# Kernel tuning notes

Measured on AMD Instinct MI355X. Metric: run time of the kernel, lower is better.

The kernel has to match this reference:

```python
import jax, jax.numpy as jnp
import numpy as np

N_NODES = 50000
N_EDGES = 800000
F_IN = 64
HID = 64
N_CLASSES = 10
N_GRAPHS = 64


def setup_inputs() -> dict:
    key = jax.random.key(0)
    ks = jax.random.split(key, 16)
    x = jax.random.normal(ks[0], (N_NODES, F_IN), dtype=jnp.float32)
    edge_index = jax.random.randint(ks[1], (2, N_EDGES), 0, N_NODES, dtype=jnp.int32)
    supernode_mask = jax.random.bernoulli(ks[2], 0.1, (N_NODES,))
    edge_mask = jax.random.bernoulli(ks[3], 0.5, (N_EDGES,)).astype(jnp.float32)
    batch = jnp.sort(jax.random.randint(ks[4], (N_NODES,), 0, N_GRAPHS, dtype=jnp.int32))
    def glorot(k, fan_in, fan_out):
        s = jnp.sqrt(6.0 / (fan_in + fan_out))
        return jax.random.uniform(k, (fan_in, fan_out), jnp.float32, -s, s)
    W1 = glorot(ks[5], F_IN, HID); b1 = jnp.zeros((HID,), jnp.float32)
    W2 = glorot(ks[6], HID, HID); b2 = jnp.zeros((HID,), jnp.float32)
    W3 = glorot(ks[7], HID, HID); b3 = jnp.zeros((HID,), jnp.float32)
    Wl = glorot(ks[8], HID, N_CLASSES); bl = jnp.zeros((N_CLASSES,), jnp.float32)
    return {"x": x, "edge_index": edge_index, "supernode_mask": supernode_mask,
            "edge_mask": edge_mask, "batch": batch,
            "W1": W1, "b1": b1, "W2": W2, "b2": b2, "W3": W3, "b3": b3,
            "Wl": Wl, "bl": bl}


def reference(x, edge_index, supernode_mask, edge_mask, batch,
              W1, b1, W2, b2, W3, b3, Wl, bl):
    N = x.shape[0]
    src, dst = edge_index[0], edge_index[1]

    # SimpleConv('add'): weighted sum of source features into targets
    x2 = jax.ops.segment_sum(x[src] * edge_mask[:, None], dst, num_segments=N)
    x = jnp.where(supernode_mask[:, None], x2, x)

    # GCN normalization with self-loops: deg = 1 + in-degree, norm = d^-1/2[src]*d^-1/2[dst]
    deg = jax.ops.segment_sum(jnp.ones((src.shape[0],), x.dtype), dst, num_segments=N) + 1.0
    dinv = jax.lax.rsqrt(deg)
    coef = dinv[src] * dinv[dst]          # [E]
    self_coef = (dinv * dinv)[:, None]    # self-loop contribution [N,1]

    def gcn(h, W, b):
        h = h @ W  # small GEMM [N, HID]
        agg = jax.ops.segment_sum(h[src] * coef[:, None], dst, num_segments=N)
        return agg + h * self_coef + b

    h = jax.nn.relu(gcn(x, W1, b1))
    h = jax.nn.relu(gcn(h, W2, b2))
    h = gcn(h, W3, b3)

    # global_mean_pool over graphs
    sums = jax.ops.segment_sum(h, batch, num_segments=N_GRAPHS)
    cnt = jax.ops.segment_sum(jnp.ones((N,), h.dtype), batch, num_segments=N_GRAPHS)
    pooled = sums / jnp.maximum(cnt, 1.0)[:, None]

    # dropout is identity in eval mode
    return pooled @ Wl + bl
```

## Files before the change

kernel.cpp:

```cpp
#include <hip/hip_runtime.h>

#define FEAT 64
#define NGRAPH 64
#define POOL_CHUNKS 8


__device__ __forceinline__ unsigned int pack_bf16(float a, float b) {
    unsigned int ua = __float_as_uint(a), ub = __float_as_uint(b);
    ua = (ua + 0x7FFFu + ((ua >> 16) & 1u)) >> 16;
    ub = (ub + 0x7FFFu + ((ub >> 16) & 1u)) >> 16;
    return ua | (ub << 16);
}
__device__ __forceinline__ float bf_lo(unsigned int w) {
    return __uint_as_float(w << 16);
}
__device__ __forceinline__ float bf_hi(unsigned int w) {
    return __uint_as_float(w & 0xFFFF0000u);
}

__global__ __launch_bounds__(256) void k_init(int* __restrict__ cnt_int,
                                              float* __restrict__ pooled,
                                              int* __restrict__ flag, int N) {
    int i = blockIdx.x * 256 + threadIdx.x;
    if (i < N) cnt_int[i] = 0;
    if (i < NGRAPH * FEAT) pooled[i] = 0.f;
    if (i == 0) *flag = 0;
}

__global__ __launch_bounds__(256) void k_detect(const unsigned int* __restrict__ m,
                                                int nwords, int* __restrict__ flag) {
    int i = blockIdx.x * 256 + threadIdx.x;
    if (i >= nwords) return;
    unsigned int w = m[i];
    if (w == 0x3F800000u) atomicOr(flag, 2);
    else if (w > 1u) atomicOr(flag, 1);
}

__device__ __forceinline__ bool read_mask(const void* sm, int i, int fl) {
    if (fl & 2) return ((const float*)sm)[i] != 0.f;
    if (fl & 1) return ((const unsigned char*)sm)[i] != 0;
    return ((const int*)sm)[i] != 0;
}

__global__ __launch_bounds__(256) void k_count(const int* __restrict__ ei,
                                               int* __restrict__ cnt_int,
                                               int* __restrict__ rank, int E) {
    int e = blockIdx.x * 256 + threadIdx.x;
    if (e >= E) return;
    rank[e] = atomicAdd(&cnt_int[ei[E + e]], 1);
}

__global__ __launch_bounds__(256) void k_scan1(const int* __restrict__ cnt,
                                               int* __restrict__ rowptr,
                                               int* __restrict__ bsum, int N) {
    __shared__ int woff[4];
    int t = threadIdx.x, lane = t & 63, wid = t >> 6;
    int i = blockIdx.x * 256 + t;
    int orig = (i < N) ? cnt[i] : 0;
    int v = orig;
#pragma unroll
    for (int off = 1; off < 64; off <<= 1) {
        int u = __shfl_up(v, off);
        if (lane >= off) v += u;
    }
    if (lane == 63) woff[wid] = v;
    __syncthreads();
    if (t == 0) {
        int a = 0;
#pragma unroll
        for (int w = 0; w < 4; ++w) { int b = woff[w]; woff[w] = a; a += b; }
    }
    __syncthreads();
    int excl = woff[wid] + v - orig;
    if (i < N) rowptr[i] = excl;
    if (t == 255) bsum[blockIdx.x] = woff[3] + v;
}

__global__ __launch_bounds__(256) void k_scan2(int* __restrict__ bsum, int nb) {
    __shared__ int woff[4];
    int t = threadIdx.x, lane = t & 63, wid = t >> 6;
    int orig = (t < nb) ? bsum[t] : 0;
    int v = orig;
#pragma unroll
    for (int off = 1; off < 64; off <<= 1) {
        int u = __shfl_up(v, off);
        if (lane >= off) v += u;
    }
    if (lane == 63) woff[wid] = v;
    __syncthreads();
    if (t == 0) {
        int a = 0;
#pragma unroll
        for (int w = 0; w < 4; ++w) { int b = woff[w]; woff[w] = a; a += b; }
    }
    __syncthreads();
    if (t < nb) bsum[t] = woff[wid] + v - orig;
}

__global__ __launch_bounds__(256) void k_scan3(const int* __restrict__ cnt,
                                               const int* __restrict__ bsum,
                                               int* __restrict__ rowptr,
                                               float* __restrict__ dinv,
                                               int N, int E) {
    int i = blockIdx.x * 256 + threadIdx.x;
    if (i >= N) return;
    rowptr[i] += bsum[blockIdx.x];
    dinv[i] = rsqrtf((float)cnt[i] + 1.0f);
    if (i == 0) rowptr[N] = E;
}

__global__ __launch_bounds__(256) void k_fill(const int* __restrict__ ei,
                                              const float* __restrict__ emask,
                                              const int* __restrict__ rowptr,
                                              const int* __restrict__ rank,
                                              unsigned int* __restrict__ csr, int E) {
    int e = blockIdx.x * 256 + threadIdx.x;
    if (e >= E) return;
    int dst = ei[E + e];
    unsigned int word = (unsigned int)ei[e];
    if (emask[e] != 0.f) word |= 0x10000u;
    csr[rowptr[dst] + rank[e]] = word;
}

__global__ __launch_bounds__(256) void k_sup(const float* __restrict__ x,
                                             const int* __restrict__ rowptr,
                                             const unsigned int* __restrict__ csr,
                                             const void* __restrict__ sm,
                                             const int* __restrict__ flag,
                                             float* __restrict__ xbuf, int N) {
    int t = blockIdx.x * 256 + threadIdx.x;
    int i = t >> 6, lane = t & 63;
    if (i >= N) return;
    int g = lane >> 4, q = lane & 15;
    int fl = *flag;
    if (read_mask(sm, i, fl)) {
        int r0 = rowptr[i], r1 = rowptr[i + 1];
        float4 acc = {0.f, 0.f, 0.f, 0.f};
        for (int j0 = r0; j0 < r1; j0 += 64) {
            int cnt = min(64, r1 - j0);
            unsigned int w_l = (lane < cnt) ? csr[j0 + lane] : 0u;
            int rounds4 = (cnt + 3) & ~3;
#pragma unroll 2
            for (int j = 0; j < rounds4; j += 4) {
                unsigned int wd = __shfl(w_l, j + g);
                if (wd & 0x10000u) {
                    int s = (int)(wd & 0xFFFFu);
                    const float4 v = *(const float4*)(x + (size_t)s * FEAT + q * 4);
                    acc.x += v.x; acc.y += v.y; acc.z += v.z; acc.w += v.w;
                }
            }
        }
#pragma unroll
        for (int m = 16; m < 64; m <<= 1) {
            acc.x += __shfl_xor(acc.x, m);
            acc.y += __shfl_xor(acc.y, m);
            acc.z += __shfl_xor(acc.z, m);
            acc.w += __shfl_xor(acc.w, m);
        }
        if (g == 0)
            *(float4*)(xbuf + (size_t)i * FEAT + q * 4) = acc;
    } else if (g == 0) {
        const float4 v = *(const float4*)(x + (size_t)i * FEAT + q * 4);
        *(float4*)(xbuf + (size_t)i * FEAT + q * 4) = v;
    }
}

__global__ __launch_bounds__(256) void k_gemm(const float* __restrict__ in,
                                              const float* __restrict__ W,
                                              const float* __restrict__ dinv,
                                              unsigned int* __restrict__ hd, int N) {
    __shared__ float wl[64 * 64];
    __shared__ float xl[16 * 68];
    int t = threadIdx.x;
    int row0 = blockIdx.x * 16;
#pragma unroll
    for (int i = 0; i < 16; ++i) wl[t + i * 256] = W[t + i * 256];
    int r = t >> 4, c = t & 15;
    int row = row0 + r;
    if (row < N)
        *(float4*)(xl + r * 68 + c * 4) = *(const float4*)(in + row * 64 + c * 4);
    __syncthreads();
    if (row >= N) return;
    float4 acc = {0.f, 0.f, 0.f, 0.f};
#pragma unroll
    for (int k = 0; k < 64; ++k) {
        float xv = xl[r * 68 + k];
        const float4 wv = *(const float4*)(wl + k * 64 + c * 4);
        acc.x += xv * wv.x;
        acc.y += xv * wv.y;
        acc.z += xv * wv.z;
        acc.w += xv * wv.w;
    }
    float di = dinv[row];
    uint2 p;
    p.x = pack_bf16(acc.x * di, acc.y * di);
    p.y = pack_bf16(acc.z * di, acc.w * di);
    *(uint2*)(hd + (size_t)row * 32 + c * 2) = p;
}

__global__ __launch_bounds__(256) void k_gather(const unsigned int* __restrict__ hd,
                                                const float* __restrict__ b,
                                                const float* __restrict__ dinv,
                                                const int* __restrict__ rowptr,
                                                const unsigned int* __restrict__ csr,
                                                float* __restrict__ out,
                                                int N, int do_relu) {
    int t = blockIdx.x * 256 + threadIdx.x;
    int i = t >> 6, lane = t & 63;
    if (i >= N) return;
    int g = lane >> 4, q = lane & 15;
    int r0 = rowptr[i], r1 = rowptr[i + 1];
    float4 acc = {0.f, 0.f, 0.f, 0.f};
    for (int j0 = r0; j0 < r1; j0 += 64) {
        int cnt = min(64, r1 - j0);
        int s_l = (lane < cnt) ? (int)(csr[j0 + lane] & 0xFFFFu) : 0;
        int rounds4 = (cnt + 3) & ~3;
#pragma unroll 4
        for (int j = 0; j < rounds4; j += 4) {
            int jj = j + g;
            int s = __shfl(s_l, jj);
            if (jj < cnt) {
                const uint2 v = *(const uint2*)(hd + (size_t)s * 32 + q * 2);
                acc.x += bf_lo(v.x); acc.y += bf_hi(v.x);
                acc.z += bf_lo(v.y); acc.w += bf_hi(v.y);
            }
        }
    }
#pragma unroll
    for (int m = 16; m < 64; m <<= 1) {
        acc.x += __shfl_xor(acc.x, m);
        acc.y += __shfl_xor(acc.y, m);
        acc.z += __shfl_xor(acc.z, m);
        acc.w += __shfl_xor(acc.w, m);
    }
    if (g == 0) {
        float dd = dinv[i];
        const uint2 hv = *(const uint2*)(hd + (size_t)i * 32 + q * 2);
        const float4 bv = *(const float4*)(b + q * 4);
        float4 r;
        r.x = (acc.x + bf_lo(hv.x)) * dd + bv.x;
        r.y = (acc.y + bf_hi(hv.x)) * dd + bv.y;
        r.z = (acc.z + bf_lo(hv.y)) * dd + bv.z;
        r.w = (acc.w + bf_hi(hv.y)) * dd + bv.w;
        if (do_relu) {
            r.x = fmaxf(r.x, 0.f); r.y = fmaxf(r.y, 0.f);
            r.z = fmaxf(r.z, 0.f); r.w = fmaxf(r.w, 0.f);
        }
        *(float4*)(out + (size_t)i * FEAT + q * 4) = r;
    }
}

__device__ __forceinline__ int lbound(const int* a, int n, int key) {
    int lo = 0, hi = n;
    while (lo < hi) {
        int mid = (lo + hi) >> 1;
        if (a[mid] < key) lo = mid + 1; else hi = mid;
    }
    return lo;
}

__global__ __launch_bounds__(256) void k_pool(const float* __restrict__ xbuf,
                                              const int* __restrict__ batch,
                                              float* __restrict__ pooled,
                                              float* __restrict__ gcnt, int N) {
    int g = blockIdx.x >> 3, c = blockIdx.x & (POOL_CHUNKS - 1);
    int lo = lbound(batch, N, g);
    int hi = lbound(batch, N, g + 1);
    int len = hi - lo;
    int t = threadIdx.x, lane = t & 63, sub = t >> 6;
    if (c == 0 && t == 0) gcnt[g] = (float)len;
    int a = lo + (int)(((long long)len * c) / POOL_CHUNKS);
    int bnd = lo + (int)(((long long)len * (c + 1)) / POOL_CHUNKS);
    float s = 0.f;
    for (int i = a + sub; i < bnd; i += 4) s += xbuf[(size_t)i * FEAT + lane];
    __shared__ float red[4][64];
    red[sub][lane] = s;
    __syncthreads();
    if (sub == 0) {
        float tot = red[0][lane] + red[1][lane] + red[2][lane] + red[3][lane];
        unsafeAtomicAdd(&pooled[g * FEAT + lane], tot);
    }
}

__global__ __launch_bounds__(640) void k_logits(const float* __restrict__ pooled,
                                                const float* __restrict__ gcnt,
                                                const float* __restrict__ Wl,
                                                const float* __restrict__ bl,
                                                float* __restrict__ out) {
    int t = threadIdx.x;
    if (t >= NGRAPH * 10) return;
    int g = t / 10, cls = t % 10;
    float inv = 1.f / fmaxf(gcnt[g], 1.f);
    float s = 0.f;
#pragma unroll
    for (int f = 0; f < 64; ++f) s += pooled[g * 64 + f] * Wl[f * 10 + cls];
    out[t] = s * inv + bl[cls];
}

extern "C" void kernel_launch(void* const* d_in, const int* in_sizes, int n_in,
                              void* d_out, int out_size, void* d_ws, size_t ws_size,
                              hipStream_t stream) {
    const float* x = (const float*)d_in[0];
    const int* ei = (const int*)d_in[1];
    const void* sm = d_in[2];
    const float* emask = (const float*)d_in[3];
    const int* batch = (const int*)d_in[4];
    const float* W1 = (const float*)d_in[5];
    const float* b1 = (const float*)d_in[6];
    const float* W2 = (const float*)d_in[7];
    const float* b2 = (const float*)d_in[8];
    const float* W3 = (const float*)d_in[9];
    const float* b3 = (const float*)d_in[10];
    const float* Wl = (const float*)d_in[11];
    const float* bl = (const float*)d_in[12];

    const int N = in_sizes[0] / FEAT;
    const int E = in_sizes[1] / 2;

    float* wsf = (float*)d_ws;
    size_t off = 0;
    float* xbuf = wsf + off;          off += (size_t)N * FEAT;
    unsigned int* hd = (unsigned int*)(wsf + off); off += (size_t)N * 32;
    int* rowptr = (int*)(wsf + off);  off += N + 1;
    int* rank = (int*)(wsf + off);    off += E;
    int* cnt_int = (int*)(wsf + off); off += N;
    float* dinv = wsf + off;          off += N;
    int* bsum = (int*)(wsf + off);    off += 256;
    unsigned int* csr = (unsigned int*)(wsf + off); off += E;
    float* pooled = wsf + off;        off += NGRAPH * FEAT;
    float* gcnt = wsf + off;          off += NGRAPH;
    int* flag = (int*)(wsf + off);

    const int nblocks = (N + 255) / 256;
    const int eblocks = (E + 255) / 256;
    const int wblocks = (N * 64 + 255) / 256;
    const int gemm_blocks = (N + 15) / 16;
    const int detect_blocks = (N / 4 + 255) / 256;

    k_init<<<nblocks, 256, 0, stream>>>(cnt_int, pooled, flag, N);
    k_detect<<<detect_blocks, 256, 0, stream>>>((const unsigned int*)sm, N / 4, flag);
    k_count<<<eblocks, 256, 0, stream>>>(ei, cnt_int, rank, E);
    k_scan1<<<nblocks, 256, 0, stream>>>(cnt_int, rowptr, bsum, N);
    k_scan2<<<1, 256, 0, stream>>>(bsum, nblocks);
    k_scan3<<<nblocks, 256, 0, stream>>>(cnt_int, bsum, rowptr, dinv, N, E);
    k_fill<<<eblocks, 256, 0, stream>>>(ei, emask, rowptr, rank, csr, E);
    k_sup<<<wblocks, 256, 0, stream>>>(x, rowptr, csr, sm, flag, xbuf, N);

    k_gemm<<<gemm_blocks, 256, 0, stream>>>(xbuf, W1, dinv, hd, N);
    k_gather<<<wblocks, 256, 0, stream>>>(hd, b1, dinv, rowptr, csr, xbuf, N, 1);
    k_gemm<<<gemm_blocks, 256, 0, stream>>>(xbuf, W2, dinv, hd, N);
    k_gather<<<wblocks, 256, 0, stream>>>(hd, b2, dinv, rowptr, csr, xbuf, N, 1);
    k_gemm<<<gemm_blocks, 256, 0, stream>>>(xbuf, W3, dinv, hd, N);
    k_gather<<<wblocks, 256, 0, stream>>>(hd, b3, dinv, rowptr, csr, xbuf, N, 0);

    k_pool<<<NGRAPH * POOL_CHUNKS, 256, 0, stream>>>(xbuf, batch, pooled, gcnt, N);
    k_logits<<<1, 640, 0, stream>>>(pooled, gcnt, Wl, bl, (float*)d_out);
}
```

Baseline: 224.9 us.

## Fuse GEMM into gather by aggregating before transform, persistent layer kernel

Uses linearity, A(XW) = (AX)W, to aggregate dinv-scaled bf16 features first and then multiply by W inside the same kernel, with W held in registers per lane. This removes the three separate GEMM kernels and their intermediate round-trips through global memory. The supernode kernel now writes dinv-scaled bf16 input directly, and each layer's output is written as the next layer's prescaled bf16 input. Layers run as a grid-stride persistent kernel with 2048 blocks. The 64-float register array per lane raises register pressure, and the final matvec for every node goes through LDS.

```diff
diff --git a/kernel.cpp b/kernel.cpp
--- a/kernel.cpp
+++ b/kernel.cpp
@@ -3,6 +3,7 @@
 #define FEAT 64
 #define NGRAPH 64
 #define POOL_CHUNKS 8
+#define LAYER_BLOCKS 2048
 
 
 __device__ __forceinline__ unsigned int pack_bf16(float a, float b) {
@@ -127,15 +128,17 @@
                                              const unsigned int* __restrict__ csr,
                                              const void* __restrict__ sm,
                                              const int* __restrict__ flag,
-                                             float* __restrict__ xbuf, int N) {
+                                             const float* __restrict__ dinv,
+                                             unsigned int* __restrict__ u, int N) {
     int t = blockIdx.x * 256 + threadIdx.x;
     int i = t >> 6, lane = t & 63;
     if (i >= N) return;
     int g = lane >> 4, q = lane & 15;
     int fl = *flag;
+    float4 acc;
     if (read_mask(sm, i, fl)) {
         int r0 = rowptr[i], r1 = rowptr[i + 1];
-        float4 acc = {0.f, 0.f, 0.f, 0.f};
+        acc.x = 0.f; acc.y = 0.f; acc.z = 0.f; acc.w = 0.f;
         for (int j0 = r0; j0 < r1; j0 += 64) {
             int cnt = min(64, r1 - j0);
             unsigned int w_l = (lane < cnt) ? csr[j0 + lane] : 0u;
@@ -157,96 +160,83 @@
             acc.z += __shfl_xor(acc.z, m);
             acc.w += __shfl_xor(acc.w, m);
         }
-        if (g == 0)
-            *(float4*)(xbuf + (size_t)i * FEAT + q * 4) = acc;
-    } else if (g == 0) {
-        const float4 v = *(const float4*)(x + (size_t)i * FEAT + q * 4);
-        *(float4*)(xbuf + (size_t)i * FEAT + q * 4) = v;
-    }
-}
-
-__global__ __launch_bounds__(256) void k_gemm(const float* __restrict__ in,
-                                              const float* __restrict__ W,
-                                              const float* __restrict__ dinv,
-                                              unsigned int* __restrict__ hd, int N) {
-    __shared__ float wl[64 * 64];
-    __shared__ float xl[16 * 68];
-    int t = threadIdx.x;
-    int row0 = blockIdx.x * 16;
-#pragma unroll
-    for (int i = 0; i < 16; ++i) wl[t + i * 256] = W[t + i * 256];
-    int r = t >> 4, c = t & 15;
-    int row = row0 + r;
-    if (row < N)
-        *(float4*)(xl + r * 68 + c * 4) = *(const float4*)(in + row * 64 + c * 4);
-    __syncthreads();
-    if (row >= N) return;
-    float4 acc = {0.f, 0.f, 0.f, 0.f};
-#pragma unroll
-    for (int k = 0; k < 64; ++k) {
-        float xv = xl[r * 68 + k];
-        const float4 wv = *(const float4*)(wl + k * 64 + c * 4);
-        acc.x += xv * wv.x;
-        acc.y += xv * wv.y;
-        acc.z += xv * wv.z;
-        acc.w += xv * wv.w;
-    }
-    float di = dinv[row];
-    uint2 p;
-    p.x = pack_bf16(acc.x * di, acc.y * di);
-    p.y = pack_bf16(acc.z * di, acc.w * di);
-    *(uint2*)(hd + (size_t)row * 32 + c * 2) = p;
-}
-
-__global__ __launch_bounds__(256) void k_gather(const unsigned int* __restrict__ hd,
-                                                const float* __restrict__ b,
-                                                const float* __restrict__ dinv,
-                                                const int* __restrict__ rowptr,
-                                                const unsigned int* __restrict__ csr,
-                                                float* __restrict__ out,
-                                                int N, int do_relu) {
-    int t = blockIdx.x * 256 + threadIdx.x;
-    int i = t >> 6, lane = t & 63;
-    if (i >= N) return;
-    int g = lane >> 4, q = lane & 15;
-    int r0 = rowptr[i], r1 = rowptr[i + 1];
-    float4 acc = {0.f, 0.f, 0.f, 0.f};
-    for (int j0 = r0; j0 < r1; j0 += 64) {
-        int cnt = min(64, r1 - j0);
-        int s_l = (lane < cnt) ? (int)(csr[j0 + lane] & 0xFFFFu) : 0;
-        int rounds4 = (cnt + 3) & ~3;
-#pragma unroll 4
-        for (int j = 0; j < rounds4; j += 4) {
-            int jj = j + g;
-            int s = __shfl(s_l, jj);
-            if (jj < cnt) {
-                const uint2 v = *(const uint2*)(hd + (size_t)s * 32 + q * 2);
-                acc.x += bf_lo(v.x); acc.y += bf_hi(v.x);
-                acc.z += bf_lo(v.y); acc.w += bf_hi(v.y);
-            }
-        }
-    }
-#pragma unroll
-    for (int m = 16; m < 64; m <<= 1) {
-        acc.x += __shfl_xor(acc.x, m);
-        acc.y += __shfl_xor(acc.y, m);
-        acc.z += __shfl_xor(acc.z, m);
-        acc.w += __shfl_xor(acc.w, m);
+    } else {
+        acc = *(const float4*)(x + (size_t)i * FEAT + q * 4);
     }
     if (g == 0) {
         float dd = dinv[i];
-        const uint2 hv = *(const uint2*)(hd + (size_t)i * 32 + q * 2);
-        const float4 bv = *(const float4*)(b + q * 4);
-        float4 r;
-        r.x = (acc.x + bf_lo(hv.x)) * dd + bv.x;
-        r.y = (acc.y + bf_hi(hv.x)) * dd + bv.y;
-        r.z = (acc.z + bf_lo(hv.y)) * dd + bv.z;
-        r.w = (acc.w + bf_hi(hv.y)) * dd + bv.w;
-        if (do_relu) {
-            r.x = fmaxf(r.x, 0.f); r.y = fmaxf(r.y, 0.f);
-            r.z = fmaxf(r.z, 0.f); r.w = fmaxf(r.w, 0.f);
-        }
-        *(float4*)(out + (size_t)i * FEAT + q * 4) = r;
+        uint2 p;
+        p.x = pack_bf16(acc.x * dd, acc.y * dd);
+        p.y = pack_bf16(acc.z * dd, acc.w * dd);
+        *(uint2*)(u + (size_t)i * 32 + q * 2) = p;
+    }
+}
+
+__global__ __launch_bounds__(256, 4) void k_layer(const unsigned int* __restrict__ u,
+                                                  const float* __restrict__ W,
+                                                  const float* __restrict__ bias,
+                                                  const float* __restrict__ dinv,
+                                                  const int* __restrict__ rowptr,
+                                                  const unsigned int* __restrict__ csr,
+                                                  unsigned int* __restrict__ u_out,
+                                                  float* __restrict__ h_out,
+                                                  int N, int mode) {
+    __shared__ float s_lds[4][64];
+    int t = threadIdx.x, lane = t & 63, wid = t >> 6;
+    int g = lane >> 4, q = lane & 15;
+    float w[64];
+#pragma unroll
+    for (int k = 0; k < 64; ++k) w[k] = W[k * 64 + lane];
+    float bl_ = bias[lane];
+    for (int i = blockIdx.x * 4 + wid; i < N; i += LAYER_BLOCKS * 4) {
+        int r0 = rowptr[i], r1 = rowptr[i + 1];
+        float4 acc = {0.f, 0.f, 0.f, 0.f};
+        if (g == 0) {
+            const uint2 v = *(const uint2*)(u + (size_t)i * 32 + q * 2);
+            acc.x += bf_lo(v.x); acc.y += bf_hi(v.x);
+            acc.z += bf_lo(v.y); acc.w += bf_hi(v.y);
+        }
+        for (int j0 = r0; j0 < r1; j0 += 64) {
+            int cnt = min(64, r1 - j0);
+            int s_l = (lane < cnt) ? (int)(csr[j0 + lane] & 0xFFFFu) : 0;
+            int rounds4 = (cnt + 3) & ~3;
+#pragma unroll 4
+            for (int j = 0; j < rounds4; j += 4) {
+                int jj = j + g;
+                int s = __shfl(s_l, jj);
+                if (jj < cnt) {
+                    const uint2 v = *(const uint2*)(u + (size_t)s * 32 + q * 2);
+                    acc.x += bf_lo(v.x); acc.y += bf_hi(v.x);
+                    acc.z += bf_lo(v.y); acc.w += bf_hi(v.y);
+                }
+            }
+        }
+#pragma unroll
+        for (int m = 16; m < 64; m <<= 1) {
+            acc.x += __shfl_xor(acc.x, m);
+            acc.y += __shfl_xor(acc.y, m);
+            acc.z += __shfl_xor(acc.z, m);
+            acc.w += __shfl_xor(acc.w, m);
+        }
+        if (g == 0) *(float4*)(&s_lds[wid][q * 4]) = acc;
+        float y = 0.f;
+#pragma unroll
+        for (int k4 = 0; k4 < 16; ++k4) {
+            const float4 sv = *(const float4*)(&s_lds[wid][k4 * 4]);
+            y += sv.x * w[k4 * 4 + 0] + sv.y * w[k4 * 4 + 1] +
+                 sv.z * w[k4 * 4 + 2] + sv.w * w[k4 * 4 + 3];
+        }
+        float dd = dinv[i];
+        y = y * dd + bl_;
+        if (mode == 0) {
+            y = fmaxf(y, 0.f);
+            float up = y * dd;
+            float other = __shfl_xor(up, 1);
+            if ((lane & 1) == 0)
+                u_out[(size_t)i * 32 + (lane >> 1)] = pack_bf16(up, other);
+        } else {
+            h_out[(size_t)i * FEAT + lane] = y;
+        }
     }
 }
 
@@ -320,7 +310,8 @@
     float* wsf = (float*)d_ws;
     size_t off = 0;
     float* xbuf = wsf + off;          off += (size_t)N * FEAT;
-    unsigned int* hd = (unsigned int*)(wsf + off); off += (size_t)N * 32;
+    unsigned int* u = (unsigned int*)(wsf + off);  off += (size_t)N * 32;
+    unsigned int* u2 = (unsigned int*)(wsf + off); off += (size_t)N * 32;
     int* rowptr = (int*)(wsf + off);  off += N + 1;
     int* rank = (int*)(wsf + off);    off += E;
     int* cnt_int = (int*)(wsf + off); off += N;
@@ -334,7 +325,6 @@
     const int nblocks = (N + 255) / 256;
     const int eblocks = (E + 255) / 256;
     const int wblocks = (N * 64 + 255) / 256;
-    const int gemm_blocks = (N + 15) / 16;
     const int detect_blocks = (N / 4 + 255) / 256;
 
     k_init<<<nblocks, 256, 0, stream>>>(cnt_int, pooled, flag, N);
@@ -344,14 +334,14 @@
     k_scan2<<<1, 256, 0, stream>>>(bsum, nblocks);
     k_scan3<<<nblocks, 256, 0, stream>>>(cnt_int, bsum, rowptr, dinv, N, E);
     k_fill<<<eblocks, 256, 0, stream>>>(ei, emask, rowptr, rank, csr, E);
-    k_sup<<<wblocks, 256, 0, stream>>>(x, rowptr, csr, sm, flag, xbuf, N);
-
-    k_gemm<<<gemm_blocks, 256, 0, stream>>>(xbuf, W1, dinv, hd, N);
-    k_gather<<<wblocks, 256, 0, stream>>>(hd, b1, dinv, rowptr, csr, xbuf, N, 1);
-    k_gemm<<<gemm_blocks, 256, 0, stream>>>(xbuf, W2, dinv, hd, N);
-    k_gather<<<wblocks, 256, 0, stream>>>(hd, b2, dinv, rowptr, csr, xbuf, N, 1);
-    k_gemm<<<gemm_blocks, 256, 0, stream>>>(xbuf, W3, dinv, hd, N);
-    k_gather<<<wblocks, 256, 0, stream>>>(hd, b3, dinv, rowptr, csr, xbuf, N, 0);
+    k_sup<<<wblocks, 256, 0, stream>>>(x, rowptr, csr, sm, flag, dinv, u, N);
+
+    k_layer<<<LAYER_BLOCKS, 256, 0, stream>>>(u, W1, b1, dinv, rowptr, csr,
+                                              u2, (float*)nullptr, N, 0);
+    k_layer<<<LAYER_BLOCKS, 256, 0, stream>>>(u2, W2, b2, dinv, rowptr, csr,
+                                              u, (float*)nullptr, N, 0);
+    k_layer<<<LAYER_BLOCKS, 256, 0, stream>>>(u, W3, b3, dinv, rowptr, csr,
+                                              (unsigned int*)nullptr, xbuf, N, 1);
 
     k_pool<<<NGRAPH * POOL_CHUNKS, 256, 0, stream>>>(xbuf, batch, pooled, gcnt, N);
     k_logits<<<1, 640, 0, stream>>>(pooled, gcnt, Wl, bl, (float*)d_out);
```

Result: slower. 239.4 us (+6.4%).
